# Kernel optimization log

Hardware: AMD Instinct MI355X
Metric: run time of the kernel (lower is better)

Reference implementation:

```python
import jax, jax.numpy as jnp
import numpy as np

H = 512  # hidden_size == input_size

def _lstm_dir(x, Wih, Whh, bih, bhh):
    # x: [B,T,H]; Wih/Whh: [4H,H]; biases: [4H]. PyTorch gate order: i,f,g,o.
    B, T, _ = x.shape
    # Precompute input contribution for all timesteps at once (one big GEMM).
    xg = jnp.einsum('bth,gh->btg', x, Wih) + bih + bhh  # [B,T,4H]
    xg = jnp.transpose(xg, (1, 0, 2))  # [T,B,4H] for scan

    def step(carry, xg_t):
        h, c = carry
        gates = xg_t + h @ Whh.T  # [B,4H]
        i, f, g, o = jnp.split(gates, 4, axis=-1)
        i = jax.nn.sigmoid(i)
        f = jax.nn.sigmoid(f)
        g = jnp.tanh(g)
        o = jax.nn.sigmoid(o)
        c = f * c + i * g
        h = o * jnp.tanh(c)
        return (h, c), h

    h0 = jnp.zeros((B, H), dtype=x.dtype)
    c0 = jnp.zeros((B, H), dtype=x.dtype)
    _, hs = jax.lax.scan(step, (h0, c0), xg)  # hs: [T,B,H]
    return jnp.transpose(hs, (1, 0, 2))  # [B,T,H]


def setup_inputs() -> dict:
    key = jax.random.key(0)
    ks = jax.random.split(key, 9)
    B, T = 32, 512
    s = 1.0 / np.sqrt(H)  # PyTorch LSTM init: U(-1/sqrt(H), 1/sqrt(H))
    u = lambda k, shape: jax.random.uniform(k, shape, jnp.float32, -s, s)
    return {
        'x': jax.random.normal(ks[0], (B, T, H), jnp.float32),
        'Wih_f': u(ks[1], (4 * H, H)), 'Whh_f': u(ks[2], (4 * H, H)),
        'bih_f': u(ks[3], (4 * H,)),   'bhh_f': u(ks[4], (4 * H,)),
        'Wih_b': u(ks[5], (4 * H, H)), 'Whh_b': u(ks[6], (4 * H, H)),
        'bih_b': u(ks[7], (4 * H,)),   'bhh_b': u(ks[8], (4 * H,)),
    }


def reference(x, Wih_f, Whh_f, bih_f, bhh_f, Wih_b, Whh_b, bih_b, bhh_b):
    fwd = _lstm_dir(x, Wih_f, Whh_f, bih_f, bhh_f)
    bwd = _lstm_dir(x[:, ::-1, :], Wih_b, Whh_b, bih_b, bhh_b)[:, ::-1, :]
    return jnp.concatenate([fwd, bwd], axis=-1)  # [B,T,2H]
```

## Files before the change

### kernel.cpp

```cpp
#include <hip/hip_runtime.h>
#include <hip/hip_bf16.h>


#define HDIM 512
#define TDIM 512
#define BDIM 32
#define NWG  64
#define NTHR 256
#define CSTRIDE 16
#define FLAGN 64
#define SLOTS (TDIM + 1)

typedef float f32x4 __attribute__((ext_vector_type(4)));
typedef _Float16 half8 __attribute__((ext_vector_type(8)));
typedef unsigned long long u64x2 __attribute__((ext_vector_type(2)));

#define SLICE_INTS (BDIM * HDIM / 2)

__device__ __forceinline__ float sigm(float x) { return 1.f / (1.f + __expf(-x)); }
__device__ __forceinline__ float tanh_f(float x) { return 1.f - 2.f / (__expf(2.f * x) + 1.f); }

__global__ void init_ws_kernel(int* __restrict__ sync, int* __restrict__ hbuf_i,
                               int nzero) {
  int i = blockIdx.x * blockDim.x + threadIdx.x;
  int n = blockDim.x * gridDim.x;
  for (int j = i; j < nzero; j += n)
    __hip_atomic_store(sync + j, 0, __ATOMIC_RELAXED, __HIP_MEMORY_SCOPE_AGENT);
  for (int j = i; j < 2 * SLICE_INTS; j += n)
    __hip_atomic_store(hbuf_i + j, 0, __ATOMIC_RELAXED, __HIP_MEMORY_SCOPE_AGENT);
}

__global__ __launch_bounds__(NTHR, 1)
void xg_gemm(const float* __restrict__ x,
             const float* __restrict__ WihF, const float* __restrict__ bihF,
             const float* __restrict__ bhhF,
             const float* __restrict__ WihB, const float* __restrict__ bihB,
             const float* __restrict__ bhhB,
             _Float16* __restrict__ xg) {
  const int blk = blockIdx.x;
  const int mb = blk & 127;
  const int ndb = blk >> 7;
  const int d = ndb >> 4;
  const int nb = ndb & 15;
  const float* Wih = d ? WihB : WihF;
  const float* bih = d ? bihB : bihF;
  const float* bhh = d ? bhhB : bhhF;
  const int mbase = mb * 128;
  const int nbase = nb * 128;

  __shared__ _Float16 As[128][40];
  __shared__ _Float16 Bs[128][40];

  const int tid = threadIdx.x;
  const int lane = tid & 63;
  const int wv = tid >> 6;
  const int wm = wv >> 1, wn = wv & 1;
  const int ln = lane & 15, quad = lane >> 4;

  f32x4 acc[4][4];
#pragma unroll
  for (int i = 0; i < 4; ++i)
#pragma unroll
    for (int j = 0; j < 4; ++j) acc[i][j] = (f32x4){0.f, 0.f, 0.f, 0.f};

  const int srow = tid >> 1, shalf = tid & 1;

  for (int kt = 0; kt < 16; ++kt) {
    const float* pa = x + (size_t)(mbase + srow) * 512 + kt * 32 + shalf * 16;
    const float* pb = Wih + (size_t)(nbase + srow) * 512 + kt * 32 + shalf * 16;
    f32x4 a0 = ((const f32x4*)pa)[0], a1 = ((const f32x4*)pa)[1];
    f32x4 a2 = ((const f32x4*)pa)[2], a3 = ((const f32x4*)pa)[3];
    f32x4 b0 = ((const f32x4*)pb)[0], b1 = ((const f32x4*)pb)[1];
    f32x4 b2 = ((const f32x4*)pb)[2], b3 = ((const f32x4*)pb)[3];
    half8 alo, ahi, blo, bhi;
#pragma unroll
    for (int j = 0; j < 4; ++j) {
      alo[j] = (_Float16)a0[j]; alo[4 + j] = (_Float16)a1[j];
      ahi[j] = (_Float16)a2[j]; ahi[4 + j] = (_Float16)a3[j];
      blo[j] = (_Float16)b0[j]; blo[4 + j] = (_Float16)b1[j];
      bhi[j] = (_Float16)b2[j]; bhi[4 + j] = (_Float16)b3[j];
    }
    __syncthreads();
    *(half8*)&As[srow][shalf * 16] = alo;
    *(half8*)&As[srow][shalf * 16 + 8] = ahi;
    *(half8*)&Bs[srow][shalf * 16] = blo;
    *(half8*)&Bs[srow][shalf * 16 + 8] = bhi;
    __syncthreads();

    half8 af[4], bf[4];
#pragma unroll
    for (int i = 0; i < 4; ++i) {
      af[i] = *(const half8*)&As[wm * 64 + i * 16 + ln][quad * 8];
      bf[i] = *(const half8*)&Bs[wn * 64 + i * 16 + ln][quad * 8];
    }
#pragma unroll
    for (int i = 0; i < 4; ++i)
#pragma unroll
      for (int j = 0; j < 4; ++j)
        acc[i][j] = __builtin_amdgcn_mfma_f32_16x16x32_f16(af[i], bf[j], acc[i][j], 0, 0, 0);
  }

  _Float16* xgd = xg + (size_t)d * 512 * 32 * 2048;
#pragma unroll
  for (int j = 0; j < 4; ++j) {
    const int n = nbase + wn * 64 + j * 16 + ln;
    const float bs = bih[n] + bhh[n];
#pragma unroll
    for (int i = 0; i < 4; ++i) {
#pragma unroll
      for (int r = 0; r < 4; ++r) {
        const int m = mbase + wm * 64 + i * 16 + quad * 4 + r;
        const int t = m & 511;
        const int b = m >> 9;
        xgd[(((size_t)t * 32 + b) * 2048) + n] = (_Float16)(acc[i][j][r] + bs);
      }
    }
  }
}

__global__ __launch_bounds__(NTHR, 1)
void lstm_rec(const float* __restrict__ WhhF, const float* __restrict__ WhhB,
              float* __restrict__ out, int* __restrict__ sync,
              int* __restrict__ hbuf, const _Float16* __restrict__ xg) {
  const int blk = blockIdx.x;
  const int d = blk & 1;
  const int w = blk >> 1;
  const int tid = threadIdx.x;
  const int lane = tid & 63;
  const int wv = tid >> 6;
  const int nt = wv & 1;
  const int mt = wv >> 1;
  const float* Whh = d ? WhhB : WhhF;

  const int nn = lane & 15;
  const int quad = lane >> 4;
  const int gg = nn & 3;
  const int jj = nt * 4 + (nn >> 2);
  const int gc = gg * HDIM + w * 8 + jj;
  const int b0 = mt * 16 + quad * 4;

  half8 whhf[16];
#pragma unroll
  for (int kbi = 0; kbi < 16; ++kbi) {
    const int k0 = kbi * 32 + quad * 8;
    const f32x4* ph = (const f32x4*)(Whh + (size_t)gc * HDIM + k0);
    f32x4 h0 = ph[0], h1 = ph[1];
    half8 b;
#pragma unroll
    for (int j = 0; j < 4; ++j) { b[j] = (_Float16)h0[j]; b[4 + j] = (_Float16)h1[j]; }
    whhf[kbi] = b;
  }

  const _Float16* xgd = xg + (size_t)d * 512 * 32 * 2048;
  const int tstep = d ? -1 : 1;
  int tx = d ? (TDIM - 1) : 0;

  _Float16 xh0, xh1, xh2, xh3;
  {
    const _Float16* xp = xgd + ((size_t)tx * 32 + b0) * 2048 + gc;
    xh0 = xp[0]; xh1 = xp[2048]; xh2 = xp[4096]; xh3 = xp[6144];
  }

  float c0 = 0.f, c1 = 0.f, c2 = 0.f, c3 = 0.f;

  for (int s = 0; s < TDIM; ++s, tx += tstep) {
    f32x4 acc = {(float)xh0, (float)xh1, (float)xh2, (float)xh3};

    if (s > 0) {
      if (wv == 0) {
        const int* pf = sync + (size_t)(d * SLOTS + s) * FLAGN + lane;
        while (__hip_atomic_load(pf, __ATOMIC_RELAXED, __HIP_MEMORY_SCOPE_AGENT) == 0) {}
      }
      __syncthreads();
    }

    const _Float16* hb = (const _Float16*)(hbuf + ((size_t)s * 2 + d) * SLICE_INTS);
#pragma unroll
    for (int kbi = 0; kbi < 16; ++kbi) {
      const int k0 = kbi * 32 + quad * 8;
      half8 a = *(const half8*)(hb + (mt * 16 + nn) * HDIM + k0);
      acc = __builtin_amdgcn_mfma_f32_16x16x32_f16(a, whhf[kbi], acc, 0, 0, 0);
    }

    float h0f, h1f, h2f, h3f;
    {
      float g0, g1, g2, g3, t1, t2;
#define CELL(R, CR, HF)                                                     \
      g0 = acc[R];                                                          \
      t1 = __shfl_xor(acc[R], 1);                                           \
      t2 = __shfl_xor(acc[R], 2);                                           \
      g3 = __shfl_xor(t1, 2);                                               \
      g1 = t1; g2 = t2;                                                     \
      {                                                                     \
        const float iv = sigm(g0), fv = sigm(g1);                           \
        const float gv = tanh_f(g2), ov = sigm(g3);                         \
        CR = fv * CR + iv * gv;                                             \
        HF = ov * tanh_f(CR);                                               \
      }
      CELL(0, c0, h0f) CELL(1, c1, h1f) CELL(2, c2, h2f) CELL(3, c3, h3f)
#undef CELL
    }

    const float hn0 = __shfl_xor(h0f, 4);
    const float hn1 = __shfl_xor(h1f, 4);
    const float hn2 = __shfl_xor(h2f, 4);
    const float hn3 = __shfl_xor(h3f, 4);
    {
      int* hw = hbuf + ((size_t)(s + 1) * 2 + d) * SLICE_INTS;
      if ((nn & 7) == 0) {
        const int colint = w * 4 + nt * 2 + (nn >> 3);
#define PUB(R, HF, HN)                                                       \
        {                                                                    \
          const unsigned lo = (unsigned)__builtin_bit_cast(unsigned short, (_Float16)(HF)); \
          const unsigned hi = (unsigned)__builtin_bit_cast(unsigned short, (_Float16)(HN)); \
          __hip_atomic_store(hw + (b0 + R) * (HDIM / 2) + colint,            \
                             (int)(lo | (hi << 16)), __ATOMIC_RELAXED,       \
                             __HIP_MEMORY_SCOPE_AGENT);                      \
        }
        PUB(0, h0f, hn0) PUB(1, h1f, hn1) PUB(2, h2f, hn2) PUB(3, h3f, hn3)
#undef PUB
      }
    }

    __syncthreads();
    if (tid == 0)
      __hip_atomic_store(sync + (size_t)(d * SLOTS + s + 1) * FLAGN + w, 1,
                         __ATOMIC_RELAXED, __HIP_MEMORY_SCOPE_AGENT);

    if (gg == 0) {
      out[((size_t)(b0 + 0) * TDIM + tx) * (2 * HDIM) + d * HDIM + w * 8 + jj] = h0f;
      out[((size_t)(b0 + 1) * TDIM + tx) * (2 * HDIM) + d * HDIM + w * 8 + jj] = h1f;
      out[((size_t)(b0 + 2) * TDIM + tx) * (2 * HDIM) + d * HDIM + w * 8 + jj] = h2f;
      out[((size_t)(b0 + 3) * TDIM + tx) * (2 * HDIM) + d * HDIM + w * 8 + jj] = h3f;
    }
    if (s + 1 < TDIM) {
      const _Float16* xp = xgd + ((size_t)(tx + tstep) * 32 + b0) * 2048 + gc;
      xh0 = xp[0]; xh1 = xp[2048]; xh2 = xp[4096]; xh3 = xp[6144];
    }
  }
}

template <int MODE>
__global__ __launch_bounds__(NTHR, 1)
void lstm_kernel(const float* __restrict__ x,
                 const float* __restrict__ WihF, const float* __restrict__ WhhF,
                 const float* __restrict__ bihF, const float* __restrict__ bhhF,
                 const float* __restrict__ WihB, const float* __restrict__ WhhB,
                 const float* __restrict__ bihB, const float* __restrict__ bhhB,
                 float* __restrict__ out,
                 int* __restrict__ sync, int* __restrict__ hbuf) {
  constexpr bool RING = (MODE < 2);
  const int blk = blockIdx.x;
  const int d = blk & 1;
  const int w = blk >> 1;
  const int tid = threadIdx.x;
  const int lane = tid & 63;
  const int wv = tid >> 6;
  const int nt = wv >> 1;
  const int kh = wv & 1;

  const float* Wih = d ? WihB : WihF;
  const float* Whh = d ? WhhB : WhhF;
  const float* bih = d ? bihB : bihF;
  const float* bhh = d ? bhhB : bhhF;

  const int nn = lane & 15;
  const int quad = lane >> 4;
  const int n32 = nt * 16 + nn;
  const int gg = n32 >> 3;
  const int jj = n32 & 7;
  const int gc = gg * HDIM + w * 8 + jj;

  half8 wihf[8], whhf[8];
#pragma unroll
  for (int kbi = 0; kbi < 8; ++kbi) {
    const int k0 = (kh * 8 + kbi) * 32 + quad * 8;
    const f32x4* pi = (const f32x4*)(Wih + (size_t)gc * HDIM + k0);
    const f32x4* ph = (const f32x4*)(Whh + (size_t)gc * HDIM + k0);
    f32x4 i0 = pi[0], i1 = pi[1], h0 = ph[0], h1 = ph[1];
    half8 a, b;
#pragma unroll
    for (int j = 0; j < 4; ++j) {
      a[j] = (_Float16)i0[j]; a[4 + j] = (_Float16)i1[j];
      b[j] = (_Float16)h0[j]; b[4 + j] = (_Float16)h1[j];
    }
    wihf[kbi] = a; whhf[kbi] = b;
  }
  const float bseed = kh ? 0.f : (bih[gc] + bhh[gc]);

  const int cb = tid >> 3;
  const int cj = tid & 7;
  const int cmt = cb >> 4;
  const int creg = cb & 3;
  const int crow = (cb & 15) >> 2;
  float c = 0.f;

  __shared__ f32x4 part[8][64];

  const int tstep = d ? -1 : 1;
  int tx = d ? (TDIM - 1) : 0;

  for (int s = 0; s < TDIM; ++s, tx += tstep) {
    f32x4 acc0 = {bseed, bseed, bseed, bseed};
    f32x4 acc1 = acc0;

#pragma unroll
    for (int kbi = 0; kbi < 8; ++kbi) {
      const int k0 = (kh * 8 + kbi) * 32 + quad * 8;
      {
        const f32x4* px = (const f32x4*)(x + ((size_t)nn * TDIM + tx) * HDIM + k0);
        f32x4 u0 = px[0], u1 = px[1];
        half8 ax;
#pragma unroll
        for (int j = 0; j < 4; ++j) { ax[j] = (_Float16)u0[j]; ax[4 + j] = (_Float16)u1[j]; }
        acc0 = __builtin_amdgcn_mfma_f32_16x16x32_f16(ax, wihf[kbi], acc0, 0, 0, 0);
      }
      {
        const f32x4* px = (const f32x4*)(x + ((size_t)(16 + nn) * TDIM + tx) * HDIM + k0);
        f32x4 u0 = px[0], u1 = px[1];
        half8 ax;
#pragma unroll
        for (int j = 0; j < 4; ++j) { ax[j] = (_Float16)u0[j]; ax[4 + j] = (_Float16)u1[j]; }
        acc1 = __builtin_amdgcn_mfma_f32_16x16x32_f16(ax, wihf[kbi], acc1, 0, 0, 0);
      }
    }

    if (s > 0) {
      if (MODE == 0) {
        if (wv == 0) {
          const int* pf = sync + (size_t)(d * SLOTS + s) * FLAGN + lane;
          while (__hip_atomic_load(pf, __ATOMIC_RELAXED, __HIP_MEMORY_SCOPE_AGENT) == 0) {}
        }
      } else {
        if (tid == 0) {
          const int* pc = sync + (size_t)(d * SLOTS + s) * CSTRIDE;
          while (__hip_atomic_load(pc, __ATOMIC_RELAXED, __HIP_MEMORY_SCOPE_AGENT) < NWG) {}
        }
      }
      __syncthreads();
    }

    if (RING) {
      const _Float16* hb =
          (const _Float16*)(hbuf + ((size_t)s * 2 + d) * SLICE_INTS);
#pragma unroll
      for (int kbi = 0; kbi < 8; ++kbi) {
        const int k0 = (kh * 8 + kbi) * 32 + quad * 8;
        half8 a0 = *(const half8*)(hb + nn * HDIM + k0);
        acc0 = __builtin_amdgcn_mfma_f32_16x16x32_f16(a0, whhf[kbi], acc0, 0, 0, 0);
        half8 a1 = *(const half8*)(hb + (16 + nn) * HDIM + k0);
        acc1 = __builtin_amdgcn_mfma_f32_16x16x32_f16(a1, whhf[kbi], acc1, 0, 0, 0);
      }
    } else {
      const unsigned long long* hb = (const unsigned long long*)(
          hbuf + ((size_t)(s & 1) * 2 + d) * SLICE_INTS);
#pragma unroll
      for (int kbi = 0; kbi < 8; ++kbi) {
        const int k0 = (kh * 8 + kbi) * 32 + quad * 8;
        {
          const unsigned long long* p = hb + (nn * (HDIM / 4) + (k0 >> 2));
          u64x2 q;
          q[0] = __hip_atomic_load(p, __ATOMIC_RELAXED, __HIP_MEMORY_SCOPE_AGENT);
          q[1] = __hip_atomic_load(p + 1, __ATOMIC_RELAXED, __HIP_MEMORY_SCOPE_AGENT);
          half8 a0 = __builtin_bit_cast(half8, q);
          acc0 = __builtin_amdgcn_mfma_f32_16x16x32_f16(a0, whhf[kbi], acc0, 0, 0, 0);
        }
        {
          const unsigned long long* p = hb + ((16 + nn) * (HDIM / 4) + (k0 >> 2));
          u64x2 q;
          q[0] = __hip_atomic_load(p, __ATOMIC_RELAXED, __HIP_MEMORY_SCOPE_AGENT);
          q[1] = __hip_atomic_load(p + 1, __ATOMIC_RELAXED, __HIP_MEMORY_SCOPE_AGENT);
          half8 a1 = __builtin_bit_cast(half8, q);
          acc1 = __builtin_amdgcn_mfma_f32_16x16x32_f16(a1, whhf[kbi], acc1, 0, 0, 0);
        }
      }
    }

    part[wv * 2 + 0][lane] = acc0;
    part[wv * 2 + 1][lane] = acc1;
    __syncthreads();

    float gv[4];
#pragma unroll
    for (int g4 = 0; g4 < 4; ++g4) {
      const int n32g = g4 * 8 + cj;
      const int ntg = n32g >> 4;
      const int ng = n32g & 15;
      const int lg = (crow << 4) | ng;
      f32x4 p0 = part[(ntg * 2 + 0) * 2 + cmt][lg];
      f32x4 p1 = part[(ntg * 2 + 1) * 2 + cmt][lg];
      gv[g4] = p0[creg] + p1[creg];
    }
    const float ig = sigm(gv[0]);
    const float fg = sigm(gv[1]);
    const float gt = tanh_f(gv[2]);
    const float og = sigm(gv[3]);
    c = fg * c + ig * gt;
    const float h = og * tanh_f(c);

    const float hn = __shfl_xor(h, 1);
    {
      const size_t tdst = RING ? (size_t)(s + 1) : (size_t)((s + 1) & 1);
      int* hw = hbuf + (tdst * 2 + d) * SLICE_INTS;
      if (!(tid & 1)) {
        const unsigned lo = (unsigned)__builtin_bit_cast(unsigned short, (_Float16)h);
        const unsigned hi = (unsigned)__builtin_bit_cast(unsigned short, (_Float16)hn);
        const int packed = (int)(lo | (hi << 16));
        __hip_atomic_store(hw + cb * (HDIM / 2) + ((w * 8 + cj) >> 1), packed,
                           __ATOMIC_RELAXED, __HIP_MEMORY_SCOPE_AGENT);
      }
    }

    __syncthreads();
    if (tid == 0) {
      if (MODE == 0) {
        __hip_atomic_store(sync + (size_t)(d * SLOTS + s + 1) * FLAGN + w, 1,
                           __ATOMIC_RELAXED, __HIP_MEMORY_SCOPE_AGENT);
      } else {
        __hip_atomic_fetch_add(sync + (size_t)(d * SLOTS + s + 1) * CSTRIDE, 1,
                               __ATOMIC_RELAXED, __HIP_MEMORY_SCOPE_AGENT);
      }
    }

    out[((size_t)cb * TDIM + tx) * (2 * HDIM) + d * HDIM + w * 8 + cj] = h;
  }
}

extern "C" void kernel_launch(void* const* d_in, const int* in_sizes, int n_in,
                              void* d_out, int out_size, void* d_ws, size_t ws_size,
                              hipStream_t stream) {
  const float* x    = (const float*)d_in[0];
  const float* WihF = (const float*)d_in[1];
  const float* WhhF = (const float*)d_in[2];
  const float* bihF = (const float*)d_in[3];
  const float* bhhF = (const float*)d_in[4];
  const float* WihB = (const float*)d_in[5];
  const float* WhhB = (const float*)d_in[6];
  const float* bihB = (const float*)d_in[7];
  const float* bhhB = (const float*)d_in[8];
  float* out = (float*)d_out;

  int* sync = (int*)d_ws;
  const size_t flag_bytes = (size_t)2 * SLOTS * FLAGN * 4;
  const size_t cnt_bytes  = (size_t)2 * SLOTS * CSTRIDE * 4;
  const size_t ring_bytes = (size_t)SLOTS * 2 * SLICE_INTS * 4;
  const size_t xg_bytes   = (size_t)2 * 512 * 32 * 2048 * 2;
  const size_t new_req = flag_bytes + ring_bytes + xg_bytes;

  if (ws_size >= new_req) {
    int* hbuf = (int*)((char*)d_ws + flag_bytes);
    _Float16* xg = (_Float16*)((char*)d_ws + flag_bytes + ring_bytes);
    hipLaunchKernelGGL(init_ws_kernel, dim3(256), dim3(NTHR), 0, stream,
                       sync, hbuf, (int)(2 * SLOTS * FLAGN));
    hipLaunchKernelGGL(xg_gemm, dim3(4096), dim3(NTHR), 0, stream,
                       x, WihF, bihF, bhhF, WihB, bihB, bhhB, xg);
    hipLaunchKernelGGL(lstm_rec, dim3(2 * NWG), dim3(NTHR), 0, stream,
                       WhhF, WhhB, out, sync, hbuf, xg);
    return;
  }

  const size_t ringF_bytes = flag_bytes + ring_bytes;
  const size_t ringC_bytes = cnt_bytes + ring_bytes;
  const int mode = (ws_size >= ringF_bytes) ? 0 : (ws_size >= ringC_bytes ? 1 : 2);
  int* hbuf = (int*)((char*)d_ws + (mode == 0 ? flag_bytes : cnt_bytes));
  const int nzero = (mode == 0) ? 2 * SLOTS * FLAGN : 2 * SLOTS * CSTRIDE;

  hipLaunchKernelGGL(init_ws_kernel, dim3(256), dim3(NTHR), 0, stream,
                     sync, hbuf, nzero);
  if (mode == 0) {
    hipLaunchKernelGGL((lstm_kernel<0>), dim3(2 * NWG), dim3(NTHR), 0, stream,
                       x, WihF, WhhF, bihF, bhhF, WihB, WhhB, bihB, bhhB,
                       out, sync, hbuf);
  } else if (mode == 1) {
    hipLaunchKernelGGL((lstm_kernel<1>), dim3(2 * NWG), dim3(NTHR), 0, stream,
                       x, WihF, WhhF, bihF, bhhF, WihB, WhhB, bihB, bhhB,
                       out, sync, hbuf);
  } else {
    hipLaunchKernelGGL((lstm_kernel<2>), dim3(2 * NWG), dim3(NTHR), 0, stream,
                       x, WihF, WhhF, bihF, bhhF, WihB, WhhB, bihB, bhhB,
                       out, sync, hbuf);
  }
}
```

Before: 2.953 ms.

## Pin recurrent LSTM workgroups to one XCC per direction and use narrower-scope stores

The recurrent kernel now launches an oversized grid. Each workgroup reads its XCC id and claims a (direction, slice) role so that all 64 workgroups of a direction sit on the same XCC, and surplus workgroups exit. When every workgroup of a direction lands on its intended XCC, the h-state publishes and step flags use workgroup-scope atomic stores instead of agent-scope ones, aiming to keep cross-workgroup exchange in the shared L2 and cut sync latency. The cost is a startup claim/spin phase with a timeout fallback, and a reliance on workgroup-scope stores being visible across CUs on the same XCC, which is a correctness risk.

```diff
diff --git a/kernel.cpp b/kernel.cpp
--- a/kernel.cpp
+++ b/kernel.cpp
@@ -7,6 +7,7 @@
 #define BDIM 32
 #define NWG  64
 #define NTHR 256
+#define GRID_REC 768
 #define CSTRIDE 16
 #define FLAGN 64
 #define SLOTS (TDIM + 1)
@@ -16,9 +17,18 @@
 typedef unsigned long long u64x2 __attribute__((ext_vector_type(2)));
 
 #define SLICE_INTS (BDIM * HDIM / 2)
+#define FLAG_INTS (2 * SLOTS * FLAGN)
+#define CLAIM_OFF FLAG_INTS
+#define XCCREC_OFF (FLAG_INTS + 16)
+#define SYNC_INTS (FLAG_INTS + 16 + 2 * NWG)
 
 __device__ __forceinline__ float sigm(float x) { return 1.f / (1.f + __expf(-x)); }
 __device__ __forceinline__ float tanh_f(float x) { return 1.f - 2.f / (__expf(2.f * x) + 1.f); }
+
+__device__ __forceinline__ void st_scoped(int* p, int v, bool fast) {
+  if (fast) __hip_atomic_store(p, v, __ATOMIC_RELAXED, __HIP_MEMORY_SCOPE_WORKGROUP);
+  else      __hip_atomic_store(p, v, __ATOMIC_RELAXED, __HIP_MEMORY_SCOPE_AGENT);
+}
 
 __global__ void init_ws_kernel(int* __restrict__ sync, int* __restrict__ hbuf_i,
                                int nzero) {
@@ -122,12 +132,58 @@
 void lstm_rec(const float* __restrict__ WhhF, const float* __restrict__ WhhB,
               float* __restrict__ out, int* __restrict__ sync,
               int* __restrict__ hbuf, const _Float16* __restrict__ xg) {
-  const int blk = blockIdx.x;
-  const int d = blk & 1;
-  const int w = blk >> 1;
   const int tid = threadIdx.x;
   const int lane = tid & 63;
   const int wv = tid >> 6;
+
+  __shared__ int srole[2];
+  __shared__ int sfast;
+  if (tid == 0) {
+    int xcc = __builtin_amdgcn_s_getreg((31 << 11) | 20) & 7;
+    int* claim = sync + CLAIM_OFF;
+    int dir = -1, role = -1;
+    if (xcc < 2) {
+      int t = __hip_atomic_fetch_add(&claim[xcc], 1, __ATOMIC_RELAXED,
+                                     __HIP_MEMORY_SCOPE_AGENT);
+      if (t < NWG) { dir = xcc; role = t; }
+    }
+    if (role < 0) {
+      const unsigned long long t0 = __builtin_amdgcn_s_memrealtime();
+      for (;;) {
+        int c0 = __hip_atomic_load(&claim[0], __ATOMIC_RELAXED, __HIP_MEMORY_SCOPE_AGENT);
+        int c1 = __hip_atomic_load(&claim[1], __ATOMIC_RELAXED, __HIP_MEMORY_SCOPE_AGENT);
+        if (c0 >= NWG && c1 >= NWG) break;
+        if (__builtin_amdgcn_s_memrealtime() - t0 > 10000) {
+          for (int dd = 0; dd < 2 && role < 0; ++dd) {
+            int t = __hip_atomic_fetch_add(&claim[dd], 1, __ATOMIC_RELAXED,
+                                           __HIP_MEMORY_SCOPE_AGENT);
+            if (t < NWG) { dir = dd; role = t; }
+          }
+          break;
+        }
+        __builtin_amdgcn_s_sleep(8);
+      }
+    }
+    srole[0] = dir; srole[1] = role;
+    if (role >= 0)
+      __hip_atomic_store(sync + XCCREC_OFF + dir * NWG + role, xcc + 1,
+                         __ATOMIC_RELAXED, __HIP_MEMORY_SCOPE_AGENT);
+  }
+  __syncthreads();
+  const int d = srole[0];
+  const int w = srole[1];
+  if (d < 0) return;
+
+  if (wv == 0) {
+    const int* px = sync + XCCREC_OFF + d * NWG + lane;
+    int v;
+    while ((v = __hip_atomic_load(px, __ATOMIC_RELAXED, __HIP_MEMORY_SCOPE_AGENT)) == 0) {}
+    const unsigned long long m = __ballot(v == d + 1);
+    if (tid == 0) sfast = (m == ~0ull) ? 1 : 0;
+  }
+  __syncthreads();
+  const bool fast = (sfast != 0);
+
   const int nt = wv & 1;
   const int mt = wv >> 1;
   const float* Whh = d ? WhhB : WhhF;
@@ -213,9 +269,8 @@
         {                                                                    \
           const unsigned lo = (unsigned)__builtin_bit_cast(unsigned short, (_Float16)(HF)); \
           const unsigned hi = (unsigned)__builtin_bit_cast(unsigned short, (_Float16)(HN)); \
-          __hip_atomic_store(hw + (b0 + R) * (HDIM / 2) + colint,            \
-                             (int)(lo | (hi << 16)), __ATOMIC_RELAXED,       \
-                             __HIP_MEMORY_SCOPE_AGENT);                      \
+          st_scoped(hw + (b0 + R) * (HDIM / 2) + colint,                     \
+                    (int)(lo | (hi << 16)), fast);                           \
         }
         PUB(0, h0f, hn0) PUB(1, h1f, hn1) PUB(2, h2f, hn2) PUB(3, h3f, hn3)
 #undef PUB
@@ -224,8 +279,7 @@
 
     __syncthreads();
     if (tid == 0)
-      __hip_atomic_store(sync + (size_t)(d * SLOTS + s + 1) * FLAGN + w, 1,
-                         __ATOMIC_RELAXED, __HIP_MEMORY_SCOPE_AGENT);
+      st_scoped(sync + (size_t)(d * SLOTS + s + 1) * FLAGN + w, 1, fast);
 
     if (gg == 0) {
       out[((size_t)(b0 + 0) * TDIM + tx) * (2 * HDIM) + d * HDIM + w * 8 + jj] = h0f;
@@ -441,20 +495,21 @@
   float* out = (float*)d_out;
 
   int* sync = (int*)d_ws;
-  const size_t flag_bytes = (size_t)2 * SLOTS * FLAGN * 4;
+  const size_t sync_bytes = (size_t)SYNC_INTS * 4;
+  const size_t flag_bytes = (size_t)FLAG_INTS * 4;
   const size_t cnt_bytes  = (size_t)2 * SLOTS * CSTRIDE * 4;
   const size_t ring_bytes = (size_t)SLOTS * 2 * SLICE_INTS * 4;
   const size_t xg_bytes   = (size_t)2 * 512 * 32 * 2048 * 2;
-  const size_t new_req = flag_bytes + ring_bytes + xg_bytes;
+  const size_t new_req = sync_bytes + ring_bytes + xg_bytes;
 
   if (ws_size >= new_req) {
-    int* hbuf = (int*)((char*)d_ws + flag_bytes);
-    _Float16* xg = (_Float16*)((char*)d_ws + flag_bytes + ring_bytes);
+    int* hbuf = (int*)((char*)d_ws + sync_bytes);
+    _Float16* xg = (_Float16*)((char*)d_ws + sync_bytes + ring_bytes);
     hipLaunchKernelGGL(init_ws_kernel, dim3(256), dim3(NTHR), 0, stream,
-                       sync, hbuf, (int)(2 * SLOTS * FLAGN));
+                       sync, hbuf, (int)SYNC_INTS);
     hipLaunchKernelGGL(xg_gemm, dim3(4096), dim3(NTHR), 0, stream,
                        x, WihF, bihF, bhhF, WihB, bihB, bhhB, xg);
-    hipLaunchKernelGGL(lstm_rec, dim3(2 * NWG), dim3(NTHR), 0, stream,
+    hipLaunchKernelGGL(lstm_rec, dim3(GRID_REC), dim3(NTHR), 0, stream,
                        WhhF, WhhB, out, sync, hbuf, xg);
     return;
   }
@@ -463,7 +518,7 @@
   const size_t ringC_bytes = cnt_bytes + ring_bytes;
   const int mode = (ws_size >= ringF_bytes) ? 0 : (ws_size >= ringC_bytes ? 1 : 2);
   int* hbuf = (int*)((char*)d_ws + (mode == 0 ? flag_bytes : cnt_bytes));
-  const int nzero = (mode == 0) ? 2 * SLOTS * FLAGN : 2 * SLOTS * CSTRIDE;
+  const int nzero = (mode == 0) ? FLAG_INTS : 2 * SLOTS * CSTRIDE;
 
   hipLaunchKernelGGL(init_ws_kernel, dim3(256), dim3(NTHR), 0, stream,
                      sync, hbuf, nzero);
```

Result: slower. 4.312 ms (+46.0%).

## Consolidate LSTM recurrence onto 16 workgroups per direction with 2x2 MFMA tiles

Applied to the files above, without the earlier changes.

Each workgroup in the recurrent kernel now owns 32 hidden units instead of 8, and each wave computes a 2x2 block of 16x16 MFMA tiles covering all 32 batch rows and two gate-column groups. The grid shrinks from 128 to 32 workgroups, so each step waits on only 16 flags, spaced apart to avoid sharing cache lines. The aim is to cut grid-wide synchronisation latency per timestep, which dominates a sequential recurrence. The cost is four times the MFMA and activation work per workgroup and twice the register-resident weights, which lengthens each step's critical path.

```diff
diff --git a/kernel.cpp b/kernel.cpp
--- a/kernel.cpp
+++ b/kernel.cpp
@@ -6,9 +6,11 @@
 #define TDIM 512
 #define BDIM 32
 #define NWG  64
+#define NW16 16
 #define NTHR 256
 #define CSTRIDE 16
 #define FLAGN 64
+#define FSTRIDE 4
 #define SLOTS (TDIM + 1)
 
 typedef float f32x4 __attribute__((ext_vector_type(4)));
@@ -16,6 +18,7 @@
 typedef unsigned long long u64x2 __attribute__((ext_vector_type(2)));
 
 #define SLICE_INTS (BDIM * HDIM / 2)
+#define FLAG_INTS (2 * SLOTS * FLAGN)
 
 __device__ __forceinline__ float sigm(float x) { return 1.f / (1.f + __expf(-x)); }
 __device__ __forceinline__ float tanh_f(float x) { return 1.f - 2.f / (__expf(2.f * x) + 1.f); }
@@ -128,47 +131,71 @@
   const int tid = threadIdx.x;
   const int lane = tid & 63;
   const int wv = tid >> 6;
-  const int nt = wv & 1;
-  const int mt = wv >> 1;
   const float* Whh = d ? WhhB : WhhF;
 
   const int nn = lane & 15;
   const int quad = lane >> 4;
   const int gg = nn & 3;
-  const int jj = nt * 4 + (nn >> 2);
-  const int gc = gg * HDIM + w * 8 + jj;
-  const int b0 = mt * 16 + quad * 4;
-
-  half8 whhf[16];
+  const int hc0 = w * 32 + wv * 8 + (nn >> 2);
+  const int gc0 = gg * HDIM + hc0;
+  const int gc1 = gc0 + 4;
+
+  half8 whh0[16], whh1[16];
 #pragma unroll
   for (int kbi = 0; kbi < 16; ++kbi) {
     const int k0 = kbi * 32 + quad * 8;
-    const f32x4* ph = (const f32x4*)(Whh + (size_t)gc * HDIM + k0);
-    f32x4 h0 = ph[0], h1 = ph[1];
-    half8 b;
-#pragma unroll
-    for (int j = 0; j < 4; ++j) { b[j] = (_Float16)h0[j]; b[4 + j] = (_Float16)h1[j]; }
-    whhf[kbi] = b;
+    {
+      const f32x4* ph = (const f32x4*)(Whh + (size_t)gc0 * HDIM + k0);
+      f32x4 h0 = ph[0], h1 = ph[1];
+      half8 b;
+#pragma unroll
+      for (int j = 0; j < 4; ++j) { b[j] = (_Float16)h0[j]; b[4 + j] = (_Float16)h1[j]; }
+      whh0[kbi] = b;
+    }
+    {
+      const f32x4* ph = (const f32x4*)(Whh + (size_t)gc1 * HDIM + k0);
+      f32x4 h0 = ph[0], h1 = ph[1];
+      half8 b;
+#pragma unroll
+      for (int j = 0; j < 4; ++j) { b[j] = (_Float16)h0[j]; b[4 + j] = (_Float16)h1[j]; }
+      whh1[kbi] = b;
+    }
   }
 
   const _Float16* xgd = xg + (size_t)d * 512 * 32 * 2048;
   const int tstep = d ? -1 : 1;
   int tx = d ? (TDIM - 1) : 0;
 
-  _Float16 xh0, xh1, xh2, xh3;
-  {
-    const _Float16* xp = xgd + ((size_t)tx * 32 + b0) * 2048 + gc;
-    xh0 = xp[0]; xh1 = xp[2048]; xh2 = xp[4096]; xh3 = xp[6144];
-  }
-
-  float c0 = 0.f, c1 = 0.f, c2 = 0.f, c3 = 0.f;
+  _Float16 xh[2][2][4];
+#pragma unroll
+  for (int mt = 0; mt < 2; ++mt)
+#pragma unroll
+    for (int r = 0; r < 4; ++r) {
+      const _Float16* xp = xgd + ((size_t)tx * 32 + mt * 16 + quad * 4 + r) * 2048;
+      xh[mt][0][r] = xp[gc0];
+      xh[mt][1][r] = xp[gc1];
+    }
+
+  float cst[2][2][4];
+#pragma unroll
+  for (int mt = 0; mt < 2; ++mt)
+#pragma unroll
+    for (int nt = 0; nt < 2; ++nt)
+#pragma unroll
+      for (int r = 0; r < 4; ++r) cst[mt][nt][r] = 0.f;
 
   for (int s = 0; s < TDIM; ++s, tx += tstep) {
-    f32x4 acc = {(float)xh0, (float)xh1, (float)xh2, (float)xh3};
+    f32x4 acc[2][2];
+#pragma unroll
+    for (int mt = 0; mt < 2; ++mt)
+#pragma unroll
+      for (int nt = 0; nt < 2; ++nt)
+        acc[mt][nt] = (f32x4){(float)xh[mt][nt][0], (float)xh[mt][nt][1],
+                              (float)xh[mt][nt][2], (float)xh[mt][nt][3]};
 
     if (s > 0) {
-      if (wv == 0) {
-        const int* pf = sync + (size_t)(d * SLOTS + s) * FLAGN + lane;
+      if (wv == 0 && lane < NW16) {
+        const int* pf = sync + (size_t)(d * SLOTS + s) * FLAGN + lane * FSTRIDE;
         while (__hip_atomic_load(pf, __ATOMIC_RELAXED, __HIP_MEMORY_SCOPE_AGENT) == 0) {}
       }
       __syncthreads();
@@ -178,64 +205,75 @@
 #pragma unroll
     for (int kbi = 0; kbi < 16; ++kbi) {
       const int k0 = kbi * 32 + quad * 8;
-      half8 a = *(const half8*)(hb + (mt * 16 + nn) * HDIM + k0);
-      acc = __builtin_amdgcn_mfma_f32_16x16x32_f16(a, whhf[kbi], acc, 0, 0, 0);
-    }
-
-    float h0f, h1f, h2f, h3f;
-    {
-      float g0, g1, g2, g3, t1, t2;
-#define CELL(R, CR, HF)                                                     \
-      g0 = acc[R];                                                          \
-      t1 = __shfl_xor(acc[R], 1);                                           \
-      t2 = __shfl_xor(acc[R], 2);                                           \
-      g3 = __shfl_xor(t1, 2);                                               \
-      g1 = t1; g2 = t2;                                                     \
-      {                                                                     \
-        const float iv = sigm(g0), fv = sigm(g1);                           \
-        const float gv = tanh_f(g2), ov = sigm(g3);                         \
-        CR = fv * CR + iv * gv;                                             \
-        HF = ov * tanh_f(CR);                                               \
-      }
-      CELL(0, c0, h0f) CELL(1, c1, h1f) CELL(2, c2, h2f) CELL(3, c3, h3f)
-#undef CELL
-    }
-
-    const float hn0 = __shfl_xor(h0f, 4);
-    const float hn1 = __shfl_xor(h1f, 4);
-    const float hn2 = __shfl_xor(h2f, 4);
-    const float hn3 = __shfl_xor(h3f, 4);
+      half8 a0 = *(const half8*)(hb + (0 * 16 + nn) * HDIM + k0);
+      half8 a1 = *(const half8*)(hb + (1 * 16 + nn) * HDIM + k0);
+      acc[0][0] = __builtin_amdgcn_mfma_f32_16x16x32_f16(a0, whh0[kbi], acc[0][0], 0, 0, 0);
+      acc[0][1] = __builtin_amdgcn_mfma_f32_16x16x32_f16(a0, whh1[kbi], acc[0][1], 0, 0, 0);
+      acc[1][0] = __builtin_amdgcn_mfma_f32_16x16x32_f16(a1, whh0[kbi], acc[1][0], 0, 0, 0);
+      acc[1][1] = __builtin_amdgcn_mfma_f32_16x16x32_f16(a1, whh1[kbi], acc[1][1], 0, 0, 0);
+    }
+
+    float hout[2][2][4];
     {
       int* hw = hbuf + ((size_t)(s + 1) * 2 + d) * SLICE_INTS;
-      if ((nn & 7) == 0) {
-        const int colint = w * 4 + nt * 2 + (nn >> 3);
-#define PUB(R, HF, HN)                                                       \
-        {                                                                    \
-          const unsigned lo = (unsigned)__builtin_bit_cast(unsigned short, (_Float16)(HF)); \
-          const unsigned hi = (unsigned)__builtin_bit_cast(unsigned short, (_Float16)(HN)); \
-          __hip_atomic_store(hw + (b0 + R) * (HDIM / 2) + colint,            \
-                             (int)(lo | (hi << 16)), __ATOMIC_RELAXED,       \
-                             __HIP_MEMORY_SCOPE_AGENT);                      \
-        }
-        PUB(0, h0f, hn0) PUB(1, h1f, hn1) PUB(2, h2f, hn2) PUB(3, h3f, hn3)
-#undef PUB
-      }
+#pragma unroll
+      for (int mt = 0; mt < 2; ++mt)
+#pragma unroll
+        for (int nt = 0; nt < 2; ++nt) {
+          const int colint = w * 16 + wv * 4 + nt * 2 + (nn >> 3);
+#pragma unroll
+          for (int r = 0; r < 4; ++r) {
+            const float g0 = acc[mt][nt][r];
+            const float t1 = __shfl_xor(g0, 1);
+            const float t2 = __shfl_xor(g0, 2);
+            const float g3 = __shfl_xor(t1, 2);
+            const float iv = sigm(g0), fv = sigm(t1);
+            const float gv = tanh_f(t2), ov = sigm(g3);
+            float c = cst[mt][nt][r];
+            c = fv * c + iv * gv;
+            cst[mt][nt][r] = c;
+            const float h = ov * tanh_f(c);
+            hout[mt][nt][r] = h;
+            const float hn = __shfl_xor(h, 4);
+            if ((nn & 7) == 0) {
+              const unsigned lo = (unsigned)__builtin_bit_cast(unsigned short, (_Float16)h);
+              const unsigned hi = (unsigned)__builtin_bit_cast(unsigned short, (_Float16)hn);
+              __hip_atomic_store(hw + (mt * 16 + quad * 4 + r) * (HDIM / 2) + colint,
+                                 (int)(lo | (hi << 16)), __ATOMIC_RELAXED,
+                                 __HIP_MEMORY_SCOPE_AGENT);
+            }
+          }
+        }
     }
 
     __syncthreads();
     if (tid == 0)
-      __hip_atomic_store(sync + (size_t)(d * SLOTS + s + 1) * FLAGN + w, 1,
+      __hip_atomic_store(sync + (size_t)(d * SLOTS + s + 1) * FLAGN + w * FSTRIDE, 1,
                          __ATOMIC_RELAXED, __HIP_MEMORY_SCOPE_AGENT);
 
     if (gg == 0) {
-      out[((size_t)(b0 + 0) * TDIM + tx) * (2 * HDIM) + d * HDIM + w * 8 + jj] = h0f;
-      out[((size_t)(b0 + 1) * TDIM + tx) * (2 * HDIM) + d * HDIM + w * 8 + jj] = h1f;
-      out[((size_t)(b0 + 2) * TDIM + tx) * (2 * HDIM) + d * HDIM + w * 8 + jj] = h2f;
-      out[((size_t)(b0 + 3) * TDIM + tx) * (2 * HDIM) + d * HDIM + w * 8 + jj] = h3f;
+#pragma unroll
+      for (int mt = 0; mt < 2; ++mt)
+#pragma unroll
+        for (int nt = 0; nt < 2; ++nt) {
+          const int hc = w * 32 + wv * 8 + nt * 4 + (nn >> 2);
+#pragma unroll
+          for (int r = 0; r < 4; ++r) {
+            const int b = mt * 16 + quad * 4 + r;
+            out[((size_t)b * TDIM + tx) * (2 * HDIM) + d * HDIM + hc] = hout[mt][nt][r];
+          }
+        }
     }
     if (s + 1 < TDIM) {
-      const _Float16* xp = xgd + ((size_t)(tx + tstep) * 32 + b0) * 2048 + gc;
-      xh0 = xp[0]; xh1 = xp[2048]; xh2 = xp[4096]; xh3 = xp[6144];
+      const int txn = tx + tstep;
+#pragma unroll
+      for (int mt = 0; mt < 2; ++mt)
+#pragma unroll
+        for (int r = 0; r < 4; ++r) {
+          const _Float16* xp = xgd + ((size_t)txn * 32 + mt * 16 + quad * 4 + r) * 2048;
+          xh[mt][0][r] = xp[gc0];
+          xh[mt][1][r] = xp[gc1];
+        }
     }
   }
 }
@@ -441,7 +479,7 @@
   float* out = (float*)d_out;
 
   int* sync = (int*)d_ws;
-  const size_t flag_bytes = (size_t)2 * SLOTS * FLAGN * 4;
+  const size_t flag_bytes = (size_t)FLAG_INTS * 4;
   const size_t cnt_bytes  = (size_t)2 * SLOTS * CSTRIDE * 4;
   const size_t ring_bytes = (size_t)SLOTS * 2 * SLICE_INTS * 4;
   const size_t xg_bytes   = (size_t)2 * 512 * 32 * 2048 * 2;
@@ -451,10 +489,10 @@
     int* hbuf = (int*)((char*)d_ws + flag_bytes);
     _Float16* xg = (_Float16*)((char*)d_ws + flag_bytes + ring_bytes);
     hipLaunchKernelGGL(init_ws_kernel, dim3(256), dim3(NTHR), 0, stream,
-                       sync, hbuf, (int)(2 * SLOTS * FLAGN));
+                       sync, hbuf, (int)FLAG_INTS);
     hipLaunchKernelGGL(xg_gemm, dim3(4096), dim3(NTHR), 0, stream,
                        x, WihF, bihF, bhhF, WihB, bihB, bhhB, xg);
-    hipLaunchKernelGGL(lstm_rec, dim3(2 * NWG), dim3(NTHR), 0, stream,
+    hipLaunchKernelGGL(lstm_rec, dim3(2 * NW16), dim3(NTHR), 0, stream,
                        WhhF, WhhB, out, sync, hbuf, xg);
     return;
   }
@@ -463,7 +501,7 @@
   const size_t ringC_bytes = cnt_bytes + ring_bytes;
   const int mode = (ws_size >= ringF_bytes) ? 0 : (ws_size >= ringC_bytes ? 1 : 2);
   int* hbuf = (int*)((char*)d_ws + (mode == 0 ? flag_bytes : cnt_bytes));
-  const int nzero = (mode == 0) ? 2 * SLOTS * FLAGN : 2 * SLOTS * CSTRIDE;
+  const int nzero = (mode == 0) ? FLAG_INTS : 2 * SLOTS * CSTRIDE;
 
   hipLaunchKernelGGL(init_ws_kernel, dim3(256), dim3(NTHR), 0, stream,
                      sync, hbuf, nzero);
```

Result: slower. 6.053 ms (+105.0%).
